# Optimization experiments

Hardware: AMD Instinct MI355X
Metric: run time of the kernel (lower is better)

Reference implementation:

```python
import jax, jax.numpy as jnp
import numpy as np

N_RAYS = 131072
N_SAMPLES = 64
N_IMPORTANCE = 128
NEAR, FAR = 2.0, 6.0


def setup_inputs() -> dict:
    key = jax.random.key(0)
    k1, k2, k3, k4 = jax.random.split(key, 4)
    rays_o = jax.random.normal(k1, (N_RAYS, 3), dtype=jnp.float32)
    rays_d = jax.random.normal(k2, (N_RAYS, 3), dtype=jnp.float32)
    # z_vals must be increasing along the sample axis (coarse sample output)
    z_vals = NEAR + (FAR - NEAR) * jnp.sort(
        jax.random.uniform(k3, (N_RAYS, N_SAMPLES), dtype=jnp.float32), axis=-1)
    weights = jax.random.uniform(k4, (N_RAYS, N_SAMPLES), dtype=jnp.float32)
    return {"rays_o": rays_o, "rays_d": rays_d, "z_vals": z_vals, "weights": weights}


def fine_sample(rays_o, rays_d, z_vals, weights):
    # z_vals: [N, S], weights: [N, S]; det=True (perturb == 0.0)
    z_mid = 0.5 * (z_vals[..., 1:] + z_vals[..., :-1])          # [N, S-1]
    w = weights[..., 1:-1] + 1e-5                               # [N, S-2]
    pdf = w / jnp.sum(w, axis=-1, keepdims=True)
    cdf = jnp.cumsum(pdf, axis=-1)
    cdf = jnp.concatenate([jnp.zeros_like(cdf[..., :1]), cdf], axis=-1)  # [N, S-1]

    u = jnp.linspace(0.0, 1.0, N_IMPORTANCE, dtype=cdf.dtype)
    u = jnp.broadcast_to(u, (cdf.shape[0], N_IMPORTANCE))       # [N, Ni]

    # per-ray binary search (right side), matching torch.searchsorted(right=True)
    inds = jax.vmap(lambda c, uu: jnp.searchsorted(c, uu, side='right'))(cdf, u)
    below = jnp.maximum(inds - 1, 0)
    above = jnp.minimum(inds, cdf.shape[-1] - 1)

    cdf_b = jnp.take_along_axis(cdf, below, axis=-1)
    cdf_a = jnp.take_along_axis(cdf, above, axis=-1)
    bins_b = jnp.take_along_axis(z_mid, below, axis=-1)
    bins_a = jnp.take_along_axis(z_mid, above, axis=-1)

    denom = cdf_a - cdf_b
    denom = jnp.where(denom < 1e-5, jnp.ones_like(denom), denom)
    t = (u - cdf_b) / denom
    z_samples = bins_b + t * (bins_a - bins_b)                  # [N, Ni]

    z_all = jnp.sort(jnp.concatenate([z_vals, z_samples], axis=-1), axis=-1)  # [N, S+Ni]
    pts = rays_o[:, None, :] + rays_d[:, None, :] * z_all[..., None]          # [N, S+Ni, 3]
    return pts, z_all


def reference(rays_o, rays_d, z_vals, weights):
    return fine_sample(rays_o, rays_d, z_vals, weights)
```

## Files before the change

kernel.cpp:

```cpp
#include <hip/hip_runtime.h>

#define S    64
#define NI   128
#define NT   192
#define WPB  4

__device__ __forceinline__ void wave_lds_fence() {
    asm volatile("s_waitcnt lgkmcnt(0)" ::: "memory");
    __builtin_amdgcn_sched_barrier(0);
}

__global__ __launch_bounds__(256) void nerf_fine_sample(
    const float* __restrict__ rays_o,
    const float* __restrict__ rays_d,
    const float* __restrict__ z_vals,
    const float* __restrict__ weights,
    float* __restrict__ out_pts,
    float* __restrict__ out_z)
{
    const int lane = threadIdx.x & 63;
    const int w    = threadIdx.x >> 6;
    const int ray  = blockIdx.x * WPB + w;

    __shared__ float s_zall[WPB][NT];
    float* const zall = s_zall[w];

    const float zv = z_vals[(size_t)ray * S + lane];
    const float wt = weights[(size_t)ray * S + lane];

    const float ox = rays_o[(size_t)ray * 3 + 0];
    const float oy = rays_o[(size_t)ray * 3 + 1];
    const float oz = rays_o[(size_t)ray * 3 + 2];
    const float dx = rays_d[(size_t)ray * 3 + 0];
    const float dy = rays_d[(size_t)ray * 3 + 1];
    const float dz = rays_d[(size_t)ray * 3 + 2];

    const float zmid = 0.5f * (zv + __shfl_down(zv, 1));

    float v = (lane >= 1 && lane <= S - 2) ? (wt + 1e-5f) : 0.0f;
    #pragma unroll
    for (int off = 1; off < 64; off <<= 1) {
        const float n = __shfl_up(v, off);
        if (lane >= off) v += n;
    }
    const float inv = 1.0f / __shfl(v, 63);
    const float cdf = v * inv;

    float zs0 = 0.0f, zs1 = 0.0f;
    const float step = 1.0f / 127.0f;
    #pragma unroll
    for (int r = 0; r < 2; ++r) {
        const int k = lane + (r << 6);
        const float u = (k == NI - 1) ? 1.0f : (float)k * step;
        int lo = 0, hi = S - 1;
        #pragma unroll
        for (int it = 0; it < 6; ++it) {
            const int m = (lo + hi) >> 1;
            const float c = __shfl(cdf, m);
            if (c <= u) lo = m + 1; else hi = m;
        }
        const int below = (lo > 0) ? lo - 1 : 0;
        const int above = (lo < S - 2) ? lo : S - 2;
        const float cb = __shfl(cdf,  below);
        const float ca = __shfl(cdf,  above);
        const float bb = __shfl(zmid, below);
        const float ba = __shfl(zmid, above);
        float denom = ca - cb;
        if (denom < 1e-5f) denom = 1.0f;
        const float t = (u - cb) / denom;
        const float z = bb + t * (ba - bb);
        if (r == 0) zs0 = z; else zs1 = z;
    }

    {
        int lo = 0, hi = NI;
        #pragma unroll
        for (int it = 0; it < 8; ++it) {
            const int m = (lo + hi) >> 1;
            const float a  = __shfl(zs0, m & 63);
            const float b  = __shfl(zs1, m & 63);
            const float val = (m >= 64) ? b : a;
            if (lo < hi) { if (val < zv) lo = m + 1; else hi = m; }
        }
        zall[lane + lo] = zv;
    }
    #pragma unroll
    for (int r = 0; r < 2; ++r) {
        const float z = (r == 0) ? zs0 : zs1;
        int lo = 0, hi = S;
        #pragma unroll
        for (int it = 0; it < 7; ++it) {
            const int m = (lo + hi) >> 1;
            const float a = __shfl(zv, m & 63);
            if (lo < hi) { if (a <= z) lo = m + 1; else hi = m; }
        }
        zall[lane + (r << 6) + lo] = z;
    }

    wave_lds_fence();

    if (lane < NT / 4) {
        const float4 q = ((const float4*)zall)[lane];
        ((float4*)(out_z + (size_t)ray * NT))[lane] = q;
    }

    const int rem0 = lane - (lane / 3) * 3;
    float o0 = (rem0 == 0) ? ox : ((rem0 == 1) ? oy : oz);
    float o1 = (rem0 == 0) ? oy : ((rem0 == 1) ? oz : ox);
    float o2 = (rem0 == 0) ? oz : ((rem0 == 1) ? ox : oy);
    float d0 = (rem0 == 0) ? dx : ((rem0 == 1) ? dy : dz);
    float d1 = (rem0 == 0) ? dy : ((rem0 == 1) ? dz : dx);
    float d2 = (rem0 == 0) ? dz : ((rem0 == 1) ? dx : dy);
    int rem = rem0;

    float* const po = out_pts + (size_t)ray * (NT * 3);
    #pragma unroll
    for (int r = 0; r < 3; ++r) {
        const int e4 = lane + (r << 6);
        if (e4 < 144) {
            const int b = e4 << 2;
            const int s = b / 3;
            const float z0 = zall[s];
            const float z1 = zall[s + 1];
            float4 q;
            q.x = fmaf(d0, z0, o0);
            q.y = fmaf(d1, (rem == 2) ? z1 : z0, o1);
            q.z = fmaf(d2, (rem == 0) ? z0 : z1, o2);
            q.w = fmaf(d0, z1, o0);
            ((float4*)po)[e4] = q;
        }
        const float to = o0; o0 = o1; o1 = o2; o2 = to;
        const float td = d0; d0 = d1; d1 = d2; d2 = td;
        rem = (rem == 2) ? 0 : rem + 1;
    }
}

extern "C" void kernel_launch(void* const* d_in, const int* in_sizes, int n_in,
                              void* d_out, int out_size, void* d_ws, size_t ws_size,
                              hipStream_t stream) {
    const float* rays_o  = (const float*)d_in[0];
    const float* rays_d  = (const float*)d_in[1];
    const float* z_vals  = (const float*)d_in[2];
    const float* weights = (const float*)d_in[3];

    const int n_rays = in_sizes[0] / 3;
    float* out_pts = (float*)d_out;
    float* out_z   = out_pts + (size_t)n_rays * NT * 3;

    const int grid = n_rays / WPB;
    nerf_fine_sample<<<grid, 256, 0, stream>>>(rays_o, rays_d, z_vals, weights,
                                               out_pts, out_z);
}
```

Baseline: 463.6 us.

## Invert sampling: each CDF bin emits its own samples and merge positions directly

The per-sample binary searches over the CDF and the two merge binary searches are replaced by an inverse mapping. Each lane owns one CDF bin, computes from ceil(127*cdf) the range of u indices that fall into it, and generates those samples with a precomputed reciprocal denominator. It scatters them into the merged array using the count of coarse z values they pass, and coarse z positions come from the counts of preceding samples. Ray origin and direction are loaded by six lanes and broadcast with readlane instead of scalar loads in every lane. The new loop has a per-lane variable trip count, so waves diverge when one bin holds many samples, and the float rounding at bin edges may differ slightly from the searchsorted semantics.

Measured after the change: 438.9 us. -5.3%, faster.

```diff
diff --git a/kernel.cpp b/kernel.cpp
--- a/kernel.cpp
+++ b/kernel.cpp
@@ -4,6 +4,10 @@
 #define NI   128
 #define NT   192
 #define WPB  4
+
+__device__ __forceinline__ float readlane_f(float x, int l) {
+    return __int_as_float(__builtin_amdgcn_readlane(__float_as_int(x), l));
+}
 
 __device__ __forceinline__ void wave_lds_fence() {
     asm volatile("s_waitcnt lgkmcnt(0)" ::: "memory");
@@ -28,14 +32,12 @@
     const float zv = z_vals[(size_t)ray * S + lane];
     const float wt = weights[(size_t)ray * S + lane];
 
-    const float ox = rays_o[(size_t)ray * 3 + 0];
-    const float oy = rays_o[(size_t)ray * 3 + 1];
-    const float oz = rays_o[(size_t)ray * 3 + 2];
-    const float dx = rays_d[(size_t)ray * 3 + 0];
-    const float dy = rays_d[(size_t)ray * 3 + 1];
-    const float dz = rays_d[(size_t)ray * 3 + 2];
-
-    const float zmid = 0.5f * (zv + __shfl_down(zv, 1));
+    float g = 0.0f;
+    if (lane < 6)
+        g = (lane < 3) ? rays_o[(size_t)ray * 3 + lane]
+                       : rays_d[(size_t)ray * 3 + (lane - 3)];
+    const float rox = readlane_f(g, 0), roy = readlane_f(g, 1), roz = readlane_f(g, 2);
+    const float rdx = readlane_f(g, 3), rdy = readlane_f(g, 4), rdz = readlane_f(g, 5);
 
     float v = (lane >= 1 && lane <= S - 2) ? (wt + 1e-5f) : 0.0f;
     #pragma unroll
@@ -43,59 +45,47 @@
         const float n = __shfl_up(v, off);
         if (lane >= off) v += n;
     }
-    const float inv = 1.0f / __shfl(v, 63);
-    const float cdf = v * inv;
+    const float total = readlane_f(v, 63);
+    const float inv   = 1.0f / total;
+    const float cdf   = v * inv;
 
-    float zs0 = 0.0f, zs1 = 0.0f;
+    const float zvn   = __shfl_down(zv, 1);
+    const float zmid  = 0.5f * (zv + zvn);
+    const float zmidn = __shfl_down(zmid, 1);
+    const float cdfn  = __shfl_down(cdf, 1);
+
+    const float dzm = (lane >= 62) ? 0.0f : (zmidn - zmid);
+    float dn        = (lane >= 62) ? 0.0f : (cdfn - cdf);
+    if (dn < 1e-5f) dn = 1.0f;
+    const float rD = 1.0f / dn;
+
     const float step = 1.0f / 127.0f;
-    #pragma unroll
-    for (int r = 0; r < 2; ++r) {
-        const int k = lane + (r << 6);
+    int c = (int)ceilf(127.0f * cdf);
+    c = (c < 0) ? 0 : ((c > 128) ? 128 : c);
+    {
+        const float um1 = ((c - 1) >= 127) ? 1.0f : (float)(c - 1) * step;
+        const float uc  = (c >= 127)       ? 1.0f : (float)c * step;
+        if (c > 0 && um1 >= cdf)      c -= 1;
+        else if (c < 128 && uc < cdf) c += 1;
+    }
+    if (lane == 63) c = 128;
+    int kn = __shfl_down(c, 1);
+    if (lane >= 63) kn = 128;
+
+    int sumb = 0;
+    for (int k = c; k < kn; ++k) {
         const float u = (k == NI - 1) ? 1.0f : (float)k * step;
-        int lo = 0, hi = S - 1;
-        #pragma unroll
-        for (int it = 0; it < 6; ++it) {
-            const int m = (lo + hi) >> 1;
-            const float c = __shfl(cdf, m);
-            if (c <= u) lo = m + 1; else hi = m;
-        }
-        const int below = (lo > 0) ? lo - 1 : 0;
-        const int above = (lo < S - 2) ? lo : S - 2;
-        const float cb = __shfl(cdf,  below);
-        const float ca = __shfl(cdf,  above);
-        const float bb = __shfl(zmid, below);
-        const float ba = __shfl(zmid, above);
-        float denom = ca - cb;
-        if (denom < 1e-5f) denom = 1.0f;
-        const float t = (u - cb) / denom;
-        const float z = bb + t * (ba - bb);
-        if (r == 0) zs0 = z; else zs1 = z;
+        const float t = (u - cdf) * rD;
+        const float z = fmaf(t, dzm, zmid);
+        const int   b = (zvn <= z) ? 1 : 0;
+        sumb += b;
+        zall[k + lane + 1 + b] = z;
     }
 
-    {
-        int lo = 0, hi = NI;
-        #pragma unroll
-        for (int it = 0; it < 8; ++it) {
-            const int m = (lo + hi) >> 1;
-            const float a  = __shfl(zs0, m & 63);
-            const float b  = __shfl(zs1, m & 63);
-            const float val = (m >= 64) ? b : a;
-            if (lo < hi) { if (val < zv) lo = m + 1; else hi = m; }
-        }
-        zall[lane + lo] = zv;
-    }
-    #pragma unroll
-    for (int r = 0; r < 2; ++r) {
-        const float z = (r == 0) ? zs0 : zs1;
-        int lo = 0, hi = S;
-        #pragma unroll
-        for (int it = 0; it < 7; ++it) {
-            const int m = (lo + hi) >> 1;
-            const float a = __shfl(zv, m & 63);
-            if (lo < hi) { if (a <= z) lo = m + 1; else hi = m; }
-        }
-        zall[lane + (r << 6) + lo] = z;
-    }
+    const float zv0 = readlane_f(zv, 0);
+    const int   pos = (lane < 63) ? (lane + 1 + kn - sumb) : 0;
+    const float pv  = (lane < 63) ? zvn : zv0;
+    zall[pos] = pv;
 
     wave_lds_fence();
 
@@ -105,12 +95,12 @@
     }
 
     const int rem0 = lane - (lane / 3) * 3;
-    float o0 = (rem0 == 0) ? ox : ((rem0 == 1) ? oy : oz);
-    float o1 = (rem0 == 0) ? oy : ((rem0 == 1) ? oz : ox);
-    float o2 = (rem0 == 0) ? oz : ((rem0 == 1) ? ox : oy);
-    float d0 = (rem0 == 0) ? dx : ((rem0 == 1) ? dy : dz);
-    float d1 = (rem0 == 0) ? dy : ((rem0 == 1) ? dz : dx);
-    float d2 = (rem0 == 0) ? dz : ((rem0 == 1) ? dx : dy);
+    float o0 = (rem0 == 0) ? rox : ((rem0 == 1) ? roy : roz);
+    float o1 = (rem0 == 0) ? roy : ((rem0 == 1) ? roz : rox);
+    float o2 = (rem0 == 0) ? roz : ((rem0 == 1) ? rox : roy);
+    float d0 = (rem0 == 0) ? rdx : ((rem0 == 1) ? rdy : rdz);
+    float d1 = (rem0 == 0) ? rdy : ((rem0 == 1) ? rdz : rdx);
+    float d2 = (rem0 == 0) ? rdz : ((rem0 == 1) ? rdx : rdy);
     int rem = rem0;
 
     float* const po = out_pts + (size_t)ray * (NT * 3);
@@ -118,8 +108,8 @@
     for (int r = 0; r < 3; ++r) {
         const int e4 = lane + (r << 6);
         if (e4 < 144) {
-            const int b = e4 << 2;
-            const int s = b / 3;
+            const int b4 = e4 << 2;
+            const int s  = b4 / 3;
             const float z0 = zall[s];
             const float z1 = zall[s + 1];
             float4 q;
```
